# Kernel tuning notes

Hardware: AMD Instinct MI355X
Metric: run time of the kernel (lower is better)

## Reference

```python
import jax, jax.numpy as jnp
from jax import lax
import numpy as np

B, T, I, H = 4096, 16, 1024, 1024


def setup_inputs() -> dict:
    key = jax.random.key(0)
    ks = jax.random.split(key, 11)
    s_i = 1.0 / np.sqrt(I)
    s_h = 1.0 / np.sqrt(H)
    return {
        "x": jax.random.normal(ks[0], (B, T, I), dtype=jnp.float32),
        "h0": jax.random.normal(ks[1], (B, H), dtype=jnp.float32),
        "bi_h0": jax.random.normal(ks[2], (B, H), dtype=jnp.float32),
        # nn.Linear(input_size, 2*hidden): weight [2H, I], bias [2H]
        "W_izr": jax.random.uniform(ks[3], (2 * H, I), jnp.float32, -s_i, s_i),
        "b_izr": jax.random.uniform(ks[4], (2 * H,), jnp.float32, -s_i, s_i),
        "W_hzr": jax.random.uniform(ks[5], (2 * H, H), jnp.float32, -s_h, s_h),
        "b_hzr": jax.random.uniform(ks[6], (2 * H,), jnp.float32, -s_h, s_h),
        "W_it": jax.random.uniform(ks[7], (H, I), jnp.float32, -s_i, s_i),
        "b_it": jax.random.uniform(ks[8], (H,), jnp.float32, -s_i, s_i),
        "W_ht": jax.random.uniform(ks[9], (H, H), jnp.float32, -s_h, s_h),
        "b_ht": jax.random.uniform(ks[10], (H,), jnp.float32, -s_h, s_h),
    }


def reference(x, h0, bi_h0, W_izr, b_izr, W_hzr, b_hzr, W_it, b_it, W_ht, b_ht):
    # batch_first: [B,T,I] -> [T,B,I]
    xs = jnp.transpose(x, (1, 0, 2))

    def cell(h, xt):
        zr = xt @ W_izr.T + b_izr + h @ W_hzr.T + b_hzr  # [B, 2H]
        r_gate, z_gate = jnp.split(zr, 2, axis=1)        # chunk(2, dim=1)
        r = jax.nn.sigmoid(r_gate)
        z = jax.nn.sigmoid(z_gate)
        h_tilda = jnp.tanh(xt @ W_it.T + b_it + r * (h @ W_ht.T + b_ht))
        nh = z * h_tilda + (1.0 - z) * h
        return nh, nh

    _, fwd = lax.scan(cell, h0, xs)            # [T,B,H], fwd[t] = hidden after x[t]
    _, bwd = lax.scan(cell, bi_h0, xs[::-1])   # bwd[j] = hidden after x[T-1-j]
    # bi_outputs[j] = cat([outputs[(T-1-j)-16] == outputs[T-1-j] (T==16), bwd[j]])
    out = jnp.concatenate([fwd[::-1], bwd], axis=-1)  # [T,B,2H], time reversed
    return jnp.transpose(out, (1, 0, 2))  # [B,T,2H]
```

## Files before the change

### kernel.cpp

```cpp
#include <hip/hip_runtime.h>


#define BDIM 4096
#define TDIM 16
#define IDIM 1024
#define HDIM 1024

typedef __bf16 bf16;
typedef __attribute__((ext_vector_type(8))) __bf16 bf16x8;
typedef __attribute__((ext_vector_type(4))) __bf16 bf16x4;
typedef __attribute__((ext_vector_type(4))) float f32x4;

__device__ __forceinline__ void g2l16(const bf16* g, bf16* l) {
  __builtin_amdgcn_global_load_lds(
      (const __attribute__((address_space(1))) void*)g,
      (__attribute__((address_space(3))) void*)l, 16, 0, 0);
}

__device__ __forceinline__ float sigmoidf_(float x) {
  return 1.0f / (1.0f + __expf(-x));
}
__device__ __forceinline__ float tanhfast_(float x) {
  return 1.0f - 2.0f / (__expf(2.0f * x) + 1.0f);
}

template <typename CT>
__global__ __launch_bounds__(256)
void gemm_bt(const bf16* __restrict__ A, const bf16* __restrict__ B,
             CT* __restrict__ C, int M, int N, int K)
{
  __shared__ bf16 sA[128 * 64];
  __shared__ bf16 sB[128 * 64];
  const int tid  = threadIdx.x;
  const int lane = tid & 63;
  const int wm = ((tid >> 6) >> 1) * 64;
  const int wn = ((tid >> 6) & 1) * 64;
  const long bm = (long)blockIdx.y * 128;
  const long bn = (long)blockIdx.x * 128;

  f32x4 acc[4][4] = {};

  const int srow = tid >> 3;
  const int scol = (tid & 7) * 8;
  const bf16* Ab = A + bm * K;
  const bf16* Bb = B + bn * K;

  const int fm = lane & 15;
  const int fk = (lane >> 4) * 8;

  for (int k0 = 0; k0 < K; k0 += 64) {
    __syncthreads();
#pragma unroll
    for (int it = 0; it < 4; ++it) {
      const int r = it * 32 + srow;
      g2l16(Ab + (long)r * K + k0 + scol, sA + (it * 256 + tid) * 8);
      g2l16(Bb + (long)r * K + k0 + scol, sB + (it * 256 + tid) * 8);
    }
    __syncthreads();
#pragma unroll
    for (int kk = 0; kk < 2; ++kk) {
      bf16x8 af[4], bfr[4];
#pragma unroll
      for (int i = 0; i < 4; ++i) {
        af[i]  = *(const bf16x8*)(sA + (wm + i * 16 + fm) * 64 + kk * 32 + fk);
        bfr[i] = *(const bf16x8*)(sB + (wn + i * 16 + fm) * 64 + kk * 32 + fk);
      }
#pragma unroll
      for (int i = 0; i < 4; ++i)
#pragma unroll
        for (int j = 0; j < 4; ++j)
          acc[i][j] = __builtin_amdgcn_mfma_f32_16x16x32_bf16(
              af[i], bfr[j], acc[i][j], 0, 0, 0);
    }
  }

  const int rg = (lane >> 4) * 4;
  const int cg = lane & 15;
#pragma unroll
  for (int i = 0; i < 4; ++i) {
#pragma unroll
    for (int j = 0; j < 4; ++j) {
      const long row0 = bm + wm + i * 16 + rg;
      const long col  = bn + wn + j * 16 + cg;
#pragma unroll
      for (int r = 0; r < 4; ++r) {
        C[(row0 + r) * (long)N + col] = (CT)acc[i][j][r];
      }
    }
  }
}

__global__ __launch_bounds__(256)
void conv_bf16(const float* __restrict__ src, bf16* __restrict__ dst, long n4) {
  long i = (long)blockIdx.x * blockDim.x + threadIdx.x;
  if (i >= n4) return;
  f32x4 v = *(const f32x4*)(src + i * 4);
  bf16x4 o;
  o[0] = (bf16)v[0]; o[1] = (bf16)v[1]; o[2] = (bf16)v[2]; o[3] = (bf16)v[3];
  *(bf16x4*)(dst + i * 4) = o;
}

__global__ __launch_bounds__(256)
void init_h(const float* __restrict__ h0, const float* __restrict__ bih0,
            float* __restrict__ hf, bf16* __restrict__ hb) {
  const long i4 = ((long)blockIdx.x * blockDim.x + threadIdx.x) * 4;
  const long nh = (long)BDIM * HDIM;
  const float* s = (i4 < nh) ? (h0 + i4) : (bih0 + (i4 - nh));
  f32x4 v = *(const f32x4*)s;
  *(f32x4*)(hf + i4) = v;
  bf16x4 o;
  o[0] = (bf16)v[0]; o[1] = (bf16)v[1]; o[2] = (bf16)v[2]; o[3] = (bf16)v[3];
  *(bf16x4*)(hb + i4) = o;
}

__global__ __launch_bounds__(256)
void gate_step(const bf16* __restrict__ U, const float* __restrict__ Gh,
               float* __restrict__ hf, bf16* __restrict__ hb,
               const float* __restrict__ b_izr, const float* __restrict__ b_hzr,
               const float* __restrict__ b_it,  const float* __restrict__ b_ht,
               float* __restrict__ out, int s)
{
  const int m = blockIdx.x;
  const int j = threadIdx.x * 4;
  const bool fwd = (m < BDIM);
  const int b  = fwd ? m : m - BDIM;
  const int tx = fwd ? s : (TDIM - 1 - s);
  const long urow = ((long)b * TDIM + tx) * (3 * HDIM);
  const long grow = (long)m * (3 * HDIM);
  const long hrow = (long)m * HDIM;

  bf16x4 ur = *(const bf16x4*)(U + urow + j);
  bf16x4 uz = *(const bf16x4*)(U + urow + HDIM + j);
  bf16x4 ut = *(const bf16x4*)(U + urow + 2 * HDIM + j);
  f32x4 gr = *(const f32x4*)(Gh + grow + j);
  f32x4 gz = *(const f32x4*)(Gh + grow + HDIM + j);
  f32x4 gt = *(const f32x4*)(Gh + grow + 2 * HDIM + j);
  f32x4 bri = *(const f32x4*)(b_izr + j);
  f32x4 bzi = *(const f32x4*)(b_izr + HDIM + j);
  f32x4 brh = *(const f32x4*)(b_hzr + j);
  f32x4 bzh = *(const f32x4*)(b_hzr + HDIM + j);
  f32x4 bti = *(const f32x4*)(b_it + j);
  f32x4 bth = *(const f32x4*)(b_ht + j);
  f32x4 hp = *(const f32x4*)(hf + hrow + j);

  f32x4 hn;
  bf16x4 hnb;
#pragma unroll
  for (int c = 0; c < 4; ++c) {
    float r = sigmoidf_((float)ur[c] + gr[c] + bri[c] + brh[c]);
    float z = sigmoidf_((float)uz[c] + gz[c] + bzi[c] + bzh[c]);
    float ht = tanhfast_((float)ut[c] + bti[c] + r * (gt[c] + bth[c]));
    float v = z * ht + (1.0f - z) * hp[c];
    hn[c] = v;
    hnb[c] = (bf16)v;
  }
  *(f32x4*)(hf + hrow + j) = hn;
  *(bf16x4*)(hb + hrow + j) = hnb;

  float* op = fwd
      ? (out + ((long)b * TDIM + (TDIM - 1 - s)) * (2 * HDIM) + j)
      : (out + ((long)b * TDIM + s) * (2 * HDIM) + HDIM + j);
  *(f32x4*)op = hn;
}

extern "C" void kernel_launch(void* const* d_in, const int* in_sizes, int n_in,
                              void* d_out, int out_size, void* d_ws, size_t ws_size,
                              hipStream_t stream) {
  const float* x     = (const float*)d_in[0];
  const float* h0    = (const float*)d_in[1];
  const float* bih0  = (const float*)d_in[2];
  const float* W_izr = (const float*)d_in[3];
  const float* b_izr = (const float*)d_in[4];
  const float* W_hzr = (const float*)d_in[5];
  const float* b_hzr = (const float*)d_in[6];
  const float* W_it  = (const float*)d_in[7];
  const float* b_it  = (const float*)d_in[8];
  const float* W_ht  = (const float*)d_in[9];
  const float* b_ht  = (const float*)d_in[10];
  float* out = (float*)d_out;

  const long n_x  = (long)BDIM * TDIM * IDIM;
  const long n_U  = (long)BDIM * TDIM * 3 * HDIM;
  const long n_Wi = (long)3 * HDIM * IDIM;
  const long n_Wh = (long)3 * HDIM * HDIM;
  const long n_h  = (long)2 * BDIM * HDIM;
  const long n_Gh = (long)2 * BDIM * 3 * HDIM;

  bf16* x_bf = (bf16*)d_ws;
  bf16* U    = x_bf + n_x;
  bf16* Wi   = U + n_U;
  bf16* Wh   = Wi + n_Wi;
  bf16* h_bf = Wh + n_Wh;
  float* Gh  = (float*)(h_bf + n_h);
  float* h_f = Gh + n_Gh;

  conv_bf16<<<(unsigned)(n_x / 4 / 256), 256, 0, stream>>>(x, x_bf, n_x / 4);
  conv_bf16<<<(unsigned)(2 * HDIM * IDIM / 4 / 256), 256, 0, stream>>>(
      W_izr, Wi, 2L * HDIM * IDIM / 4);
  conv_bf16<<<(unsigned)(HDIM * IDIM / 4 / 256), 256, 0, stream>>>(
      W_it, Wi + 2L * HDIM * IDIM, (long)HDIM * IDIM / 4);
  conv_bf16<<<(unsigned)(2 * HDIM * HDIM / 4 / 256), 256, 0, stream>>>(
      W_hzr, Wh, 2L * HDIM * HDIM / 4);
  conv_bf16<<<(unsigned)(HDIM * HDIM / 4 / 256), 256, 0, stream>>>(
      W_ht, Wh + 2L * HDIM * HDIM, (long)HDIM * HDIM / 4);
  init_h<<<(unsigned)(n_h / 4 / 256), 256, 0, stream>>>(h0, bih0, h_f, h_bf);

  {
    dim3 g(3 * HDIM / 128, BDIM * TDIM / 128);
    gemm_bt<bf16><<<g, 256, 0, stream>>>(x_bf, Wi, U,
                                         BDIM * TDIM, 3 * HDIM, IDIM);
  }

  dim3 gs(3 * HDIM / 128, 2 * BDIM / 128);
  for (int s = 0; s < TDIM; ++s) {
    gemm_bt<float><<<gs, 256, 0, stream>>>(h_bf, Wh, Gh,
                                           2 * BDIM, 3 * HDIM, HDIM);
    gate_step<<<2 * BDIM, 256, 0, stream>>>(U, Gh, h_f, h_bf,
                                            b_izr, b_hzr, b_it, b_ht, out, s);
  }
}
```

Baseline: 3.361 ms.

## Replace 128x128 GEMM with double-buffered 256x256 tile kernel using swizzled LDS

Swaps the simple 128x128-tile bf16 MFMA GEMM for a 256x256-tile, 512-thread kernel. It double-buffers K tiles in 128KB of dynamic LDS with an XOR-swizzled layout, interleaves async global-to-LDS loads with MFMA blocks under explicit barriers and s_setprio, and remaps block IDs for L2 locality. The goal is more operand reuse per tile, hidden load latency and fewer LDS bank conflicts in both the input projection and the per-step recurrent GEMMs. In exchange it uses heavy register and LDS pressure, which limits occupancy. It also hard-codes vmcnt counts and grid-size assumptions: the grid must divide by 8 and tiles by 256.

```diff
diff --git a/kernel.cpp b/kernel.cpp
--- a/kernel.cpp
+++ b/kernel.cpp
@@ -24,68 +24,159 @@
   return 1.0f - 2.0f / (__expf(2.0f * x) + 1.0f);
 }
 
+#define GBAR()                          \
+  do {                                  \
+    __builtin_amdgcn_sched_barrier(0);  \
+    __builtin_amdgcn_s_barrier();       \
+    __builtin_amdgcn_sched_barrier(0);  \
+  } while (0)
+
+template <int MB, int NB>
+__device__ __forceinline__ void mfma_block(f32x4 (&acc)[8][4],
+                                           const bf16x8 (&a)[4][2],
+                                           const bf16x8 (&b)[2][2]) {
+#pragma unroll
+  for (int mi = 0; mi < 4; ++mi)
+#pragma unroll
+    for (int j = 0; j < 2; ++j)
+#pragma unroll
+      for (int kk = 0; kk < 2; ++kk)
+        acc[MB + mi][NB + j] = __builtin_amdgcn_mfma_f32_16x16x32_bf16(
+            a[mi][kk], b[j][kk], acc[MB + mi][NB + j], 0, 0, 0);
+}
+
 template <typename CT>
-__global__ __launch_bounds__(256)
-void gemm_bt(const bf16* __restrict__ A, const bf16* __restrict__ B,
-             CT* __restrict__ C, int M, int N, int K)
+__global__ __launch_bounds__(512, 2)
+void gemm256(const bf16* __restrict__ A, const bf16* __restrict__ B,
+             CT* __restrict__ C, int N, int K, int nxb)
 {
-  __shared__ bf16 sA[128 * 64];
-  __shared__ bf16 sB[128 * 64];
+  extern __shared__ char lds[];
   const int tid  = threadIdx.x;
   const int lane = tid & 63;
-  const int wm = ((tid >> 6) >> 1) * 64;
-  const int wn = ((tid >> 6) & 1) * 64;
-  const long bm = (long)blockIdx.y * 128;
-  const long bn = (long)blockIdx.x * 128;
-
-  f32x4 acc[4][4] = {};
-
-  const int srow = tid >> 3;
-  const int scol = (tid & 7) * 8;
+  const int wid  = tid >> 6;
+  const int wm   = wid >> 2;
+  const int wn   = wid & 3;
+
+  const int nwg = (int)gridDim.x;
+  const int lin = ((int)blockIdx.x & 7) * (nwg >> 3) + ((int)blockIdx.x >> 3);
+  const long bm = (long)(lin / nxb) * 256;
+  const long bn = (long)(lin % nxb) * 256;
+
   const bf16* Ab = A + bm * K;
   const bf16* Bb = B + bn * K;
-
-  const int fm = lane & 15;
-  const int fk = (lane >> 4) * 8;
-
-  for (int k0 = 0; k0 < K; k0 += 64) {
-    __syncthreads();
-#pragma unroll
-    for (int it = 0; it < 4; ++it) {
-      const int r = it * 32 + srow;
-      g2l16(Ab + (long)r * K + k0 + scol, sA + (it * 256 + tid) * 8);
-      g2l16(Bb + (long)r * K + k0 + scol, sB + (it * 256 + tid) * 8);
-    }
-    __syncthreads();
-#pragma unroll
-    for (int kk = 0; kk < 2; ++kk) {
-      bf16x8 af[4], bfr[4];
-#pragma unroll
-      for (int i = 0; i < 4; ++i) {
-        af[i]  = *(const bf16x8*)(sA + (wm + i * 16 + fm) * 64 + kk * 32 + fk);
-        bfr[i] = *(const bf16x8*)(sB + (wn + i * 16 + fm) * 64 + kk * 32 + fk);
-      }
-#pragma unroll
-      for (int i = 0; i < 4; ++i)
-#pragma unroll
-        for (int j = 0; j < 4; ++j)
-          acc[i][j] = __builtin_amdgcn_mfma_f32_16x16x32_bf16(
-              af[i], bfr[j], acc[i][j], 0, 0, 0);
-    }
+  const int NT = K >> 6;
+
+  const int o0 = tid * 16, o1 = o0 + 8192;
+  const bf16 *gAL0, *gAL1, *gAU0, *gAU1, *gBL0, *gBL1, *gBU0, *gBU1;
+  int dAL0, dAL1, dAU0, dAU1, dBL0, dBL1, dBU0, dBU1;
+  {
+    auto mkA = [&](int o, int up, const bf16*& g, int& d) {
+      int r  = up * 64 + ((o >> 13) & 1) * 128 + ((o >> 7) & 63);
+      int cb = (o & 127) ^ ((r & 7) << 4);
+      g = Ab + (long)r * K + (cb >> 1);
+      d = r * 128 + (o & 127);
+    };
+    auto mkB = [&](int o, int up, const bf16*& g, int& d) {
+      int r  = up * 32 + ((o >> 12) & 3) * 64 + ((o >> 7) & 31);
+      int cb = (o & 127) ^ ((r & 7) << 4);
+      g = Bb + (long)r * K + (cb >> 1);
+      d = 65536 + r * 128 + (o & 127);
+    };
+    mkA(o0, 0, gAL0, dAL0); mkA(o1, 0, gAL1, dAL1);
+    mkA(o0, 1, gAU0, dAU0); mkA(o1, 1, gAU1, dAU1);
+    mkB(o0, 0, gBL0, dBL0); mkB(o1, 0, gBL1, dBL1);
+    mkB(o0, 1, gBU0, dBU0); mkB(o1, 1, gBU1, dBU1);
+  }
+  auto STG = [&](const bf16* g, int d, int kt, int bo) {
+    g2l16(g + (kt << 6), (bf16*)(lds + bo + d));
+  };
+
+  const int fm  = lane & 15;
+  const int fkb = (lane >> 4) * 16;
+  const int key = (fm & 7) << 4;
+  const char* aB0 = lds + wm * 16384 + fm * 128 + (fkb ^ key);
+  const char* aB1 = lds + wm * 16384 + fm * 128 + ((64 + fkb) ^ key);
+  const char* bB0 = lds + 65536 + wn * 8192 + fm * 128 + (fkb ^ key);
+  const char* bB1 = lds + 65536 + wn * 8192 + fm * 128 + ((64 + fkb) ^ key);
+
+  STG(gAL0, dAL0, 0, 0);     STG(gAL1, dAL1, 0, 0);
+  STG(gAU0, dAU0, 0, 0);     STG(gAU1, dAU1, 0, 0);
+  STG(gBL0, dBL0, 0, 0);     STG(gBL1, dBL1, 0, 0);
+  STG(gBU0, dBU0, 0, 0);     STG(gBU1, dBU1, 0, 0);
+  STG(gAL0, dAL0, 1, 32768); STG(gAL1, dAL1, 1, 32768);
+  STG(gBL0, dBL0, 1, 32768); STG(gBL1, dBL1, 1, 32768);
+  STG(gBU0, dBU0, 1, 32768); STG(gBU1, dBU1, 1, 32768);
+  asm volatile("s_waitcnt vmcnt(6)" ::: "memory");
+  GBAR();
+
+  f32x4 acc[8][4] = {};
+  bf16x8 aF[4][2], bLo[2][2], bHi[2][2];
+
+  auto ktile = [&](int t, int CB, int NB) {
+#pragma unroll
+    for (int mi = 0; mi < 4; ++mi)
+#pragma unroll
+      for (int kk = 0; kk < 2; ++kk)
+        aF[mi][kk] = *(const bf16x8*)((kk ? aB1 : aB0) + CB + mi * 2048);
+#pragma unroll
+    for (int j = 0; j < 2; ++j)
+#pragma unroll
+      for (int kk = 0; kk < 2; ++kk)
+        bLo[j][kk] = *(const bf16x8*)((kk ? bB1 : bB0) + CB + j * 2048);
+    if (t + 1 < NT) { STG(gAU0, dAU0, t + 1, NB); STG(gAU1, dAU1, t + 1, NB); }
+    GBAR();
+    __builtin_amdgcn_s_setprio(1);
+    mfma_block<0, 0>(acc, aF, bLo);
+    __builtin_amdgcn_s_setprio(0);
+    GBAR();
+#pragma unroll
+    for (int j = 0; j < 2; ++j)
+#pragma unroll
+      for (int kk = 0; kk < 2; ++kk)
+        bHi[j][kk] = *(const bf16x8*)((kk ? bB1 : bB0) + CB + (2 + j) * 2048);
+    if (t + 2 < NT) { STG(gAL0, dAL0, t + 2, CB); STG(gAL1, dAL1, t + 2, CB); }
+    GBAR();
+    __builtin_amdgcn_s_setprio(1);
+    mfma_block<0, 2>(acc, aF, bHi);
+    __builtin_amdgcn_s_setprio(0);
+    GBAR();
+#pragma unroll
+    for (int mi = 0; mi < 4; ++mi)
+#pragma unroll
+      for (int kk = 0; kk < 2; ++kk)
+        aF[mi][kk] = *(const bf16x8*)((kk ? aB1 : aB0) + CB + 8192 + mi * 2048);
+    if (t + 2 < NT) { STG(gBL0, dBL0, t + 2, CB); STG(gBL1, dBL1, t + 2, CB); }
+    GBAR();
+    __builtin_amdgcn_s_setprio(1);
+    mfma_block<4, 0>(acc, aF, bLo);
+    __builtin_amdgcn_s_setprio(0);
+    GBAR();
+    if (t + 2 < NT) { STG(gBU0, dBU0, t + 2, CB); STG(gBU1, dBU1, t + 2, CB); }
+    GBAR();
+    __builtin_amdgcn_s_setprio(1);
+    mfma_block<4, 2>(acc, aF, bHi);
+    __builtin_amdgcn_s_setprio(0);
+    if (t + 2 < NT) { asm volatile("s_waitcnt vmcnt(6)" ::: "memory"); }
+    else            { asm volatile("s_waitcnt vmcnt(0)" ::: "memory"); }
+    GBAR();
+  };
+
+  for (int t = 0; t < NT; t += 2) {
+    ktile(t,     0,     32768);
+    ktile(t + 1, 32768, 0);
   }
 
   const int rg = (lane >> 4) * 4;
   const int cg = lane & 15;
 #pragma unroll
-  for (int i = 0; i < 4; ++i) {
+  for (int mi = 0; mi < 8; ++mi) {
 #pragma unroll
     for (int j = 0; j < 4; ++j) {
-      const long row0 = bm + wm + i * 16 + rg;
-      const long col  = bn + wn + j * 16 + cg;
-#pragma unroll
-      for (int r = 0; r < 4; ++r) {
-        C[(row0 + r) * (long)N + col] = (CT)acc[i][j][r];
-      }
+      const long row0 = bm + wm * 128 + mi * 16 + rg;
+      const long col  = bn + wn * 64 + j * 16 + cg;
+#pragma unroll
+      for (int r = 0; r < 4; ++r)
+        C[(row0 + r) * (long)N + col] = (CT)acc[mi][j][r];
     }
   }
 }
@@ -194,6 +285,11 @@
   float* Gh  = (float*)(h_bf + n_h);
   float* h_f = Gh + n_Gh;
 
+  (void)hipFuncSetAttribute((const void*)gemm256<bf16>,
+                            hipFuncAttributeMaxDynamicSharedMemorySize, 131072);
+  (void)hipFuncSetAttribute((const void*)gemm256<float>,
+                            hipFuncAttributeMaxDynamicSharedMemorySize, 131072);
+
   conv_bf16<<<(unsigned)(n_x / 4 / 256), 256, 0, stream>>>(x, x_bf, n_x / 4);
   conv_bf16<<<(unsigned)(2 * HDIM * IDIM / 4 / 256), 256, 0, stream>>>(
       W_izr, Wi, 2L * HDIM * IDIM / 4);
@@ -205,16 +301,13 @@
       W_ht, Wh + 2L * HDIM * HDIM, (long)HDIM * HDIM / 4);
   init_h<<<(unsigned)(n_h / 4 / 256), 256, 0, stream>>>(h0, bih0, h_f, h_bf);
 
-  {
-    dim3 g(3 * HDIM / 128, BDIM * TDIM / 128);
-    gemm_bt<bf16><<<g, 256, 0, stream>>>(x_bf, Wi, U,
-                                         BDIM * TDIM, 3 * HDIM, IDIM);
-  }
-
-  dim3 gs(3 * HDIM / 128, 2 * BDIM / 128);
+  gemm256<bf16><<<dim3((BDIM * TDIM / 256) * (3 * HDIM / 256)), dim3(512),
+                  131072, stream>>>(x_bf, Wi, U, 3 * HDIM, IDIM, 3 * HDIM / 256);
+
   for (int s = 0; s < TDIM; ++s) {
-    gemm_bt<float><<<gs, 256, 0, stream>>>(h_bf, Wh, Gh,
-                                           2 * BDIM, 3 * HDIM, HDIM);
+    gemm256<float><<<dim3((2 * BDIM / 256) * (3 * HDIM / 256)), dim3(512),
+                     131072, stream>>>(h_bf, Wh, Gh, 3 * HDIM, HDIM,
+                                       3 * HDIM / 256);
     gate_step<<<2 * BDIM, 256, 0, stream>>>(U, Gh, h_f, h_bf,
                                             b_izr, b_hzr, b_it, b_ht, out, s);
   }
```

New measurement: 2.906 ms. -13.5%, faster.
